# Performance work log

Measured on AMD Instinct MI355X. Metric: run time of the kernel, lower is better.

The kernel has to match this reference:

```python
import jax, jax.numpy as jnp
import numpy as np

N_NODES = 4096
N_EDGES = 16384
L = 512
MP_STEPS = 5
DT = 0.01


def _mlp(x, W1, b1, W2, b2):
    return jax.nn.relu(x @ W1 + b1) @ W2 + b2


def _ln(x):
    m = jnp.mean(x, axis=-1, keepdims=True)
    v = jnp.var(x, axis=-1, keepdims=True)
    return (x - m) * jax.lax.rsqrt(v + 1e-6)


_PARAM_SHAPES = [
    ("enc_e_W1", (1, L)), ("enc_e_b1", (L,)), ("enc_e_W2", (L, L)), ("enc_e_b2", (L,)),
    ("enc_n_W1", (1, L)), ("enc_n_b1", (L,)), ("enc_n_W2", (L, L)), ("enc_n_b2", (L,)),
    ("proc_e_W1", (3 * L, L)), ("proc_e_b1", (L,)), ("proc_e_W2", (L, L)), ("proc_e_b2", (L,)),
    ("proc_n_W1", (2 * L, L)), ("proc_n_b1", (L,)), ("proc_n_W2", (L, L)), ("proc_n_b2", (L,)),
    ("dec_e_W1", (L, L)), ("dec_e_b1", (L,)), ("dec_e_W2", (L, 1)), ("dec_e_b2", (1,)),
]


def setup_inputs() -> dict:
    key = jax.random.key(0)
    ks = jax.random.split(key, 3 + len(_PARAM_SHAPES))
    d = {}
    d["state"] = jax.random.normal(ks[0], (N_EDGES + N_NODES,), dtype=jnp.float32)
    d["senders"] = jax.random.randint(ks[1], (N_EDGES,), 0, N_NODES)
    d["receivers"] = jax.random.randint(ks[2], (N_EDGES,), 0, N_NODES)
    for i, (name, shp) in enumerate(_PARAM_SHAPES):
        if name.endswith(("b1", "b2")):
            d[name] = jnp.zeros(shp, dtype=jnp.float32)
        else:
            d[name] = 0.02 * jax.random.normal(ks[3 + i], shp, dtype=jnp.float32)
    return d


def _hamiltonian(x, senders, receivers,
                 enc_e_W1, enc_e_b1, enc_e_W2, enc_e_b2,
                 enc_n_W1, enc_n_b1, enc_n_W2, enc_n_b2,
                 proc_e_W1, proc_e_b1, proc_e_W2, proc_e_b2,
                 proc_n_W1, proc_n_b1, proc_n_W2, proc_n_b2,
                 dec_e_W1, dec_e_b1, dec_e_W2, dec_e_b2):
    # graph_from_state: edge scalars then node scalars
    e = x[:N_EDGES].reshape(N_EDGES, 1)
    n = x[N_EDGES:].reshape(N_NODES, 1)
    # encode (MLP + layer norm)
    eh = _ln(_mlp(e, enc_e_W1, enc_e_b1, enc_e_W2, enc_e_b2))  # [E, L]
    nh = _ln(_mlp(n, enc_n_W1, enc_n_b1, enc_n_W2, enc_n_b2))  # [N, L]
    # process: num_mp_steps of GraphNetwork-style message passing, shared params
    for _ in range(MP_STEPS):
        msg_in = jnp.concatenate([eh, nh[senders], nh[receivers]], axis=-1)  # [E, 3L]
        eh = eh + _mlp(msg_in, proc_e_W1, proc_e_b1, proc_e_W2, proc_e_b2)
        agg = jax.ops.segment_sum(eh, receivers, num_segments=N_NODES)  # [N, L]
        node_in = jnp.concatenate([nh, agg], axis=-1)  # [N, 2L]
        nh = nh + _mlp(node_in, proc_n_W1, proc_n_b1, proc_n_W2, proc_n_b2)
    # decode edges to scalars; H = sum of decoded edge energies
    dec_e = _mlp(eh, dec_e_W1, dec_e_b1, dec_e_W2, dec_e_b2)  # [E, 1]
    return jnp.sum(dec_e)


def reference(state, senders, receivers,
              enc_e_W1, enc_e_b1, enc_e_W2, enc_e_b2,
              enc_n_W1, enc_n_b1, enc_n_W2, enc_n_b2,
              proc_e_W1, proc_e_b1, proc_e_W2, proc_e_b2,
              proc_n_W1, proc_n_b1, proc_n_W2, proc_n_b2,
              dec_e_W1, dec_e_b1, dec_e_W2, dec_e_b2):
    def H_fn(x):
        return _hamiltonian(x, senders, receivers,
                            enc_e_W1, enc_e_b1, enc_e_W2, enc_e_b2,
                            enc_n_W1, enc_n_b1, enc_n_W2, enc_n_b2,
                            proc_e_W1, proc_e_b1, proc_e_W2, proc_e_b2,
                            proc_n_W1, proc_n_b1, proc_n_W2, proc_n_b2,
                            dec_e_W1, dec_e_b1, dec_e_W2, dec_e_b2)
    H, dH = jax.value_and_grad(H_fn)(state)
    # one integrator step driven by the Hamiltonian gradient (stand-in for DAE solve)
    next_state = state - DT * dH
    return next_state
```

## Files before the change

kernel.cpp:

```cpp
#include <hip/hip_runtime.h>


#define E_ROWS 16384
#define N_ROWS 4096
#define ALL_ROWS 20480
#define DT_F   0.01f

typedef unsigned char u8;
typedef unsigned short u16;
typedef __attribute__((ext_vector_type(8))) short short8v;
typedef __attribute__((ext_vector_type(4))) float f32x4;

__device__ __forceinline__ u16 f2b(float f) {
    union { float f; unsigned u; } v; v.f = f;
    unsigned r = v.u + 0x7FFF + ((v.u >> 16) & 1);
    return (u16)(r >> 16);
}
__device__ __forceinline__ float b2f(u16 u) {
    union { unsigned u; float f; } v; v.u = ((unsigned)u) << 16;
    return v.f;
}

template<int BM, int WM, int WN, int KTOT, int LDA, int LDC,
         bool ADD_C, bool GATHER2, bool BIAS, bool RELU_MASK, bool APPLY_MASK,
         bool WF32, bool WBF16, bool DUALOUT, bool ROWDOT, bool DECW2, bool BSEL>
__global__ __launch_bounds__(256)
void bgemm(const u16* __restrict__ A, const u16* __restrict__ Bt, const u16* __restrict__ Bt2,
           float* __restrict__ C, u16* __restrict__ Cb,
           const u16* __restrict__ Cinb, const float* __restrict__ bias,
           const float* __restrict__ bias2, const u16* __restrict__ G12b,
           const int* __restrict__ sidx, const int* __restrict__ ridx,
           u8* __restrict__ maskw, u16* __restrict__ C2b,
           const float* __restrict__ wvec, const float* __restrict__ wvec2,
           float* __restrict__ outp)
{
    constexpr int BN = WN * 64;
    constexpr int NA = BM / 16;
    constexpr int TC = (BM + BN) / 16;
    constexpr int PER = TC / 4;
    constexpr int NT = KTOT / 32;
    constexpr int IFRAG = BM / WM / 16;
    __shared__ u16 Ls[2][TC * 512];

    const int tid = threadIdx.x;
    const int lane = tid & 63;
    const int wv = tid >> 6;
    const int wr = wv / WN;
    const int wc = wv % WN;

    const int gx = gridDim.x;
    int id = blockIdx.y * gx + blockIdx.x;
    const int nwg = gx * gridDim.y;
    id = (id & 7) * (nwg >> 3) + (id >> 3);
    const int bx = id % gx;
    const int by = id / gx;
    const int rowBase = by * BM;
    const int colBase = bx * BN;

    const u16* BtU = Bt;
    const float* biasU = bias;
    const float* wvecU = wvec;
    if (BSEL && rowBase >= E_ROWS) { BtU = Bt2; biasU = bias2; wvecU = wvec2; }

    const int srow = lane & 15;
    const int slotk = (lane >> 4) << 3;

    const u16* srcs[PER];
    int dstoff[PER];
#pragma unroll
    for (int q = 0; q < PER; ++q) {
        const int c = wv + (q << 2);
        if (c < NA)
            srcs[q] = A + (size_t)(rowBase + c * 16 + srow) * LDA + slotk;
        else
            srcs[q] = BtU + (size_t)(colBase + (c - NA) * 16 + srow) * KTOT + slotk;
        dstoff[q] = c * 512;
    }

    f32x4 acc[IFRAG][4];
#pragma unroll
    for (int i = 0; i < IFRAG; ++i)
#pragma unroll
        for (int j = 0; j < 4; ++j)
            acc[i][j] = (f32x4){0.f, 0.f, 0.f, 0.f};

    const int fro = ((lane >> 4) << 7) + ((lane & 15) << 3);

#pragma unroll
    for (int q = 0; q < PER; ++q)
        __builtin_amdgcn_global_load_lds(
            (const __attribute__((address_space(1))) void*)srcs[q],
            (__attribute__((address_space(3))) void*)&Ls[0][dstoff[q]], 16, 0, 0);
    asm volatile("s_waitcnt vmcnt(0)" ::: "memory");
    __builtin_amdgcn_s_barrier();
    asm volatile("" ::: "memory");

#pragma unroll
    for (int t = 0; t < NT; ++t) {
        const int cur = t & 1;
        if (t + 1 < NT) {
#pragma unroll
            for (int q = 0; q < PER; ++q)
                __builtin_amdgcn_global_load_lds(
                    (const __attribute__((address_space(1))) void*)(srcs[q] + (t + 1) * 32),
                    (__attribute__((address_space(3))) void*)&Ls[cur ^ 1][dstoff[q]], 16, 0, 0);
        }
        short8v af[IFRAG], bfm[4];
#pragma unroll
        for (int i = 0; i < IFRAG; ++i)
            af[i] = *(const short8v*)&Ls[cur][((wr * IFRAG + i) << 9) + fro];
#pragma unroll
        for (int j = 0; j < 4; ++j)
            bfm[j] = *(const short8v*)&Ls[cur][((NA + (wc << 2) + j) << 9) + fro];
#pragma unroll
        for (int i = 0; i < IFRAG; ++i)
#pragma unroll
            for (int j = 0; j < 4; ++j)
                acc[i][j] = __builtin_amdgcn_mfma_f32_16x16x32_bf16(af[i], bfm[j], acc[i][j], 0, 0, 0);
        if (t + 1 < NT) {
            asm volatile("s_waitcnt vmcnt(0)" ::: "memory");
            __builtin_amdgcn_s_barrier();
            asm volatile("" ::: "memory");
        }
    }

    const int colB = colBase + wc * 64 + (lane & 15);
    const int rowB = rowBase + wr * (BM / WM) + ((lane >> 4) << 2);
    float bcol[4], wv4[4];
    if (BIAS) {
#pragma unroll
        for (int j = 0; j < 4; ++j) bcol[j] = biasU[colB + (j << 4)];
    }
    if (ROWDOT || DECW2) {
#pragma unroll
        for (int j = 0; j < 4; ++j) wv4[j] = wvecU[colB + (j << 4)];
    }
    const bool upper = DUALOUT && (colBase >= 512);
#pragma unroll
    for (int i = 0; i < IFRAG; ++i) {
#pragma unroll
        for (int r = 0; r < 4; ++r) {
            const int row = rowB + (i << 4) + r;
            int si = 0, ri = 0;
            if (GATHER2) { si = sidx[row]; ri = ridx[row]; }
            float rds = 0.f;
#pragma unroll
            for (int j = 0; j < 4; ++j) {
                const int col = colB + (j << 4);
                float v = acc[i][j][r];
                if (DUALOUT && upper) {
                    C2b[(size_t)row * 512 + (col - 512)] = f2b(v);
                    continue;
                }
                if (GATHER2) v += b2f(G12b[(size_t)si * 1024 + col]) + b2f(G12b[(size_t)ri * 1024 + 512 + col]);
                if (ADD_C) v += b2f(Cinb[(size_t)row * LDC + col]);
                if (BIAS) v += bcol[j];
                if (DECW2) {
                    Cb[(size_t)row * LDC + col] = (v > 0.f) ? f2b(wv4[j]) : (u16)0;
                    continue;
                }
                if (RELU_MASK) {
                    const u8 m = v > 0.f;
                    maskw[(size_t)row * 512 + col] = m;
                    v = m ? v : 0.f;
                }
                if (APPLY_MASK) {
                    if (!maskw[(size_t)row * 512 + col]) v = 0.f;
                }
                if (ROWDOT) rds += v * wv4[j];
                const size_t o = (size_t)row * LDC + col;
                if (WF32) C[o] = v;
                if (WBF16) Cb[o] = f2b(v);
            }
            if (ROWDOT) {
#pragma unroll
                for (int m = 1; m < 16; m <<= 1) rds += __shfl_xor(rds, m);
                if ((lane & 15) == 0) atomicAdd(outp + row, -DT_F * rds);
            }
        }
    }
}

struct WArgs {
    const float* src[10];
    u16* dstP[10];
    u16* dstT[10];
    int ldP[10], ldT[10];
};

__global__ void wcvt_kernel(WArgs a)
{
    const int i = blockIdx.z;
    const float* W = a.src[i];
    u16* P = a.dstP[i]; const int lp = a.ldP[i];
    u16* T = a.dstT[i]; const int lt = a.ldT[i];
    __shared__ u16 t[64][66];
    const int rb = blockIdx.y << 6, cb = blockIdx.x << 6;
    const int tr = threadIdx.x >> 4;
    const int tc = (threadIdx.x & 15) << 2;
#pragma unroll
    for (int rr = 0; rr < 4; ++rr) {
        const int r = tr + (rr << 4);
        const float4 v = *(const float4*)&W[(size_t)(rb + r) * 512 + cb + tc];
        ushort4 u; u.x = f2b(v.x); u.y = f2b(v.y); u.z = f2b(v.z); u.w = f2b(v.w);
        *(ushort4*)&P[(size_t)(rb + r) * lp + cb + tc] = u;
        t[r][tc] = u.x; t[r][tc + 1] = u.y; t[r][tc + 2] = u.z; t[r][tc + 3] = u.w;
    }
    __syncthreads();
#pragma unroll
    for (int rr = 0; rr < 4; ++rr) {
        const int n = tr + (rr << 4);
        ushort4 u;
        u.x = t[tc][n]; u.y = t[tc + 1][n]; u.z = t[tc + 2][n]; u.w = t[tc + 3][n];
        *(ushort4*)&T[(size_t)(cb + n) * lt + rb + tc] = u;
    }
}

__device__ void csr_build(const int* __restrict__ idx, int* __restrict__ starts,
                          int* __restrict__ eids)
{
    __shared__ int hist[4096];
    __shared__ int scanbuf[1024];
    const int t = threadIdx.x;
    for (int i = t; i < 4096; i += 1024) hist[i] = 0;
    __syncthreads();
    for (int e = t; e < 16384; e += 1024) atomicAdd(&hist[idx[e]], 1);
    __syncthreads();
    const int base = t << 2;
    const int l0 = hist[base], l1 = hist[base + 1], l2 = hist[base + 2], l3 = hist[base + 3];
    const int lsum = l0 + l1 + l2 + l3;
    scanbuf[t] = lsum;
    __syncthreads();
    for (int ofs = 1; ofs < 1024; ofs <<= 1) {
        const int v = scanbuf[t];
        const int u = (t >= ofs) ? scanbuf[t - ofs] : 0;
        __syncthreads();
        scanbuf[t] = v + u;
        __syncthreads();
    }
    const int excl = scanbuf[t] - lsum;
    const int p0 = excl, p1 = p0 + l0, p2 = p1 + l1, p3 = p2 + l2;
    starts[base] = p0; starts[base + 1] = p1; starts[base + 2] = p2; starts[base + 3] = p3;
    if (t == 0) starts[4096] = 16384;
    __syncthreads();
    hist[base] = p0; hist[base + 1] = p1; hist[base + 2] = p2; hist[base + 3] = p3;
    __syncthreads();
    for (int e = t; e < 16384; e += 1024) {
        const int pos = atomicAdd(&hist[idx[e]], 1);
        eids[pos] = e;
    }
    __syncthreads();
    for (int n = t; n < 4096; n += 1024) {
        const int s0 = starts[n], s1 = hist[n];
        for (int i = s0 + 1; i < s1; ++i) {
            const int v = eids[i];
            int j = i - 1;
            while (j >= s0 && eids[j] > v) { eids[j + 1] = eids[j]; --j; }
            eids[j + 1] = v;
        }
    }
}

__global__ __launch_bounds__(1024) void csr2_kernel(const int* __restrict__ senders,
                                                    const int* __restrict__ receivers,
                                                    int* __restrict__ sst, int* __restrict__ seid,
                                                    int* __restrict__ rst, int* __restrict__ reid)
{
    if (blockIdx.x == 0) csr_build(receivers, rst, reid);
    else                 csr_build(senders, sst, seid);
}

__global__ void init_out_kernel(const float* __restrict__ state, float* __restrict__ out)
{
    const int t = blockIdx.x * 256 + threadIdx.x;
    out[t] = state[t];
}

__global__ void seg_agg_fwd_kernel(const u16* __restrict__ ehb, const int* __restrict__ starts,
                                   const int* __restrict__ eids, const u16* __restrict__ nhb,
                                   u16* __restrict__ nagg)
{
    const int n = blockIdx.x, c = threadIdx.x;
    const int s0 = starts[n], s1 = starts[n + 1];
    float a0 = 0.f, a1 = 0.f;
    for (int i = s0; i < s1; ++i) {
        const u16* p = ehb + (size_t)eids[i] * 512;
        a0 += b2f(p[c]); a1 += b2f(p[c + 256]);
    }
    u16* d = nagg + (size_t)n * 1024;
    const u16* s = nhb + (size_t)n * 512;
    d[c] = s[c]; d[c + 256] = s[c + 256];
    d[512 + c] = f2b(a0); d[768 + c] = f2b(a1);
}

__global__ void seg_sr_bwd_kernel(const u16* __restrict__ dh1e,
                                  const int* __restrict__ sst, const int* __restrict__ seid,
                                  const int* __restrict__ rst, const int* __restrict__ reid,
                                  u16* __restrict__ SR)
{
    const int n = blockIdx.x, c = threadIdx.x;
    float a0 = 0.f, a1 = 0.f, b0 = 0.f, b1 = 0.f;
    for (int i = sst[n]; i < sst[n + 1]; ++i) {
        const u16* p = dh1e + (size_t)seid[i] * 512;
        a0 += b2f(p[c]); a1 += b2f(p[c + 256]);
    }
    for (int i = rst[n]; i < rst[n + 1]; ++i) {
        const u16* p = dh1e + (size_t)reid[i] * 512;
        b0 += b2f(p[c]); b1 += b2f(p[c + 256]);
    }
    u16* d = SR + (size_t)n * 1024;
    d[c] = f2b(a0); d[c + 256] = f2b(a1);
    d[512 + c] = f2b(b0); d[768 + c] = f2b(b1);
}

__global__ void enc_h1_kernel(const float* __restrict__ x,
                              const float* __restrict__ W1e, const float* __restrict__ b1e,
                              const float* __restrict__ W1n, const float* __restrict__ b1n,
                              u16* __restrict__ h1b, u8* __restrict__ mask)
{
    const int idx = blockIdx.x * 256 + threadIdx.x;
    const int row = idx >> 7;
    const int c = (idx & 127) << 2;
    const bool edge = row < E_ROWS;
    const float* W1 = edge ? W1e : W1n;
    const float* b1 = edge ? b1e : b1n;
    const float xv = x[row];
    const float4 w = *(const float4*)&W1[c];
    const float4 b = *(const float4*)&b1[c];
    float4 v;
    v.x = fmaf(xv, w.x, b.x); v.y = fmaf(xv, w.y, b.y);
    v.z = fmaf(xv, w.z, b.z); v.w = fmaf(xv, w.w, b.w);
    uchar4 m;
    m.x = v.x > 0.f; m.y = v.y > 0.f; m.z = v.z > 0.f; m.w = v.w > 0.f;
    v.x = m.x ? v.x : 0.f; v.y = m.y ? v.y : 0.f;
    v.z = m.z ? v.z : 0.f; v.w = m.w ? v.w : 0.f;
    const size_t o = (size_t)row * 512 + c;
    ushort4 u; u.x = f2b(v.x); u.y = f2b(v.y); u.z = f2b(v.z); u.w = f2b(v.w);
    *(ushort4*)&h1b[o] = u;
    *(uchar4*)&mask[o] = m;
}

__global__ void ln_fwd_kernel(const float* __restrict__ x, u16* __restrict__ xhat_b,
                              u16* __restrict__ xb, float* __restrict__ rstd_save)
{
    const int row = blockIdx.x, tid = threadIdx.x;
    const float* p = x + (size_t)row * 512;
    const float a = p[tid], b = p[tid + 256];
    __shared__ float s1[256], s2[256];
    s1[tid] = a + b; s2[tid] = a * a + b * b;
    __syncthreads();
    for (int d = 128; d > 0; d >>= 1) {
        if (tid < d) { s1[tid] += s1[tid + d]; s2[tid] += s2[tid + d]; }
        __syncthreads();
    }
    const float mean = s1[0] * (1.f / 512.f);
    const float var = s2[0] * (1.f / 512.f) - mean * mean;
    const float r = rsqrtf(var + 1e-6f);
    const float ya = (a - mean) * r, yb = (b - mean) * r;
    const size_t o = (size_t)row * 512 + tid;
    xhat_b[o] = f2b(ya); xhat_b[o + 256] = f2b(yb);
    xb[o] = f2b(ya); xb[o + 256] = f2b(yb);
    if (tid == 0) rstd_save[row] = r;
}

__global__ void ln_bwd_kernel(u16* __restrict__ d, const u16* __restrict__ xhat_b,
                              const float* __restrict__ rstd)
{
    const int row = blockIdx.x, tid = threadIdx.x;
    u16* p = d + (size_t)row * 512;
    const u16* xh = xhat_b + (size_t)row * 512;
    const float da = b2f(p[tid]), dbv = b2f(p[tid + 256]);
    const float xa = b2f(xh[tid]), xbv = b2f(xh[tid + 256]);
    __shared__ float s1[256], s2[256];
    s1[tid] = da + dbv; s2[tid] = da * xa + dbv * xbv;
    __syncthreads();
    for (int dd = 128; dd > 0; dd >>= 1) {
        if (tid < dd) { s1[tid] += s1[tid + dd]; s2[tid] += s2[tid + dd]; }
        __syncthreads();
    }
    const float m1 = s1[0] * (1.f / 512.f);
    const float m2 = s2[0] * (1.f / 512.f);
    const float r = rstd[row];
    p[tid] = f2b(r * (da - m1 - xa * m2));
    p[tid + 256] = f2b(r * (dbv - m1 - xbv * m2));
}

__global__ void gather_add_kernel(u16* __restrict__ dst, const u16* __restrict__ src,
                                  const int* __restrict__ idx)
{
    const int t = blockIdx.x * 256 + threadIdx.x;
    const int row = t >> 6;
    const int c = (t & 63) << 3;
    const size_t o = (size_t)row * 512 + c;
    short8v a = *(const short8v*)&dst[o];
    const short8v g = *(const short8v*)&src[(size_t)idx[row] * 512 + c];
    short8v r;
#pragma unroll
    for (int i = 0; i < 8; ++i)
        r[i] = (short)f2b(b2f((u16)a[i]) + b2f((u16)g[i]));
    *(short8v*)&dst[o] = r;
}

extern "C" void kernel_launch(void* const* d_in, const int* in_sizes, int n_in,
                              void* d_out, int out_size, void* d_ws, size_t ws_size,
                              hipStream_t stream)
{
    (void)in_sizes; (void)n_in; (void)out_size; (void)ws_size;
    const float* state     = (const float*)d_in[0];
    const int*   senders   = (const int*)d_in[1];
    const int*   receivers = (const int*)d_in[2];
    const float* enc_e_W1 = (const float*)d_in[3];
    const float* enc_e_b1 = (const float*)d_in[4];
    const float* enc_e_W2 = (const float*)d_in[5];
    const float* enc_e_b2 = (const float*)d_in[6];
    const float* enc_n_W1 = (const float*)d_in[7];
    const float* enc_n_b1 = (const float*)d_in[8];
    const float* enc_n_W2 = (const float*)d_in[9];
    const float* enc_n_b2 = (const float*)d_in[10];
    const float* pe_W1 = (const float*)d_in[11];
    const float* pe_b1 = (const float*)d_in[12];
    const float* pe_W2 = (const float*)d_in[13];
    const float* pe_b2 = (const float*)d_in[14];
    const float* pn_W1 = (const float*)d_in[15];
    const float* pn_b1 = (const float*)d_in[16];
    const float* pn_W2 = (const float*)d_in[17];
    const float* pn_b2 = (const float*)d_in[18];
    const float* de_W1 = (const float*)d_in[19];
    const float* de_b1 = (const float*)d_in[20];
    const float* de_W2 = (const float*)d_in[21];
    float* out = (float*)d_out;

    const size_t EL = (size_t)E_ROWS * 512, NL = (size_t)N_ROWS * 512;
    const size_t AL = (size_t)ALL_ROWS * 512;
    const size_t LL = 512 * 512;
    char* w = (char*)d_ws;
    size_t off = 0;
    auto carve = [&](size_t bytes) -> char* {
        char* p = w + off;
        off += (bytes + 255) & ~(size_t)255;
        return p;
    };
    u16* wb = (u16*)carve(20 * LL * 2);
    u16* WT0 = wb;           u16* WT1 = wb + LL;      u16* WT2 = wb + 2 * LL;
    u16* WT34 = wb + 3 * LL;                          u16* WT5 = wb + 5 * LL;
    u16* WT8 = wb + 6 * LL;  u16* WT9 = wb + 7 * LL;
    u16* WP0 = wb + 8 * LL;  u16* WP1 = wb + 9 * LL;  u16* WP2 = wb + 10 * LL;
    u16* WP5 = wb + 11 * LL; u16* WP8 = wb + 12 * LL; u16* WP9 = wb + 13 * LL;
    u16* WT67 = wb + 14 * LL;
    u16* WP34c = wb + 16 * LL;
    u16* WP67 = wb + 18 * LL;

    float* eh  = (float*)carve(AL * 4);
    u16* ehb   = (u16*)carve(EL * 2);
    u16* nhb   = (u16*)carve(NL * 2);
    u16* h1eb  = (u16*)carve(EL * 2);
    u16* h1nb  = (u16*)carve(NL * 2);
    u16* eh0b  = (u16*)carve(EL * 2);
    u16* nh0b  = (u16*)carve(NL * 2);
    u8* menc   = (u8*)carve(AL);
    u16* G1b   = (u16*)carve(NL * 2);
    u16* G12b  = (u16*)carve(NL * 2 * 2);
    u16* nsr   = (u16*)carve(NL * 2 * 2);
    float* rstd = (float*)carve(ALL_ROWS * 4);
    u8* mpe    = (u8*)carve(5 * EL);
    u8* mpn    = (u8*)carve(5 * NL);
    int* rst  = (int*)carve(4097 * 4);
    int* reid = (int*)carve(16384 * 4);
    int* sst  = (int*)carve(4097 * 4);
    int* seid = (int*)carve(16384 * 4);

    const dim3 blk(256);
    const dim3 gE(4, E_ROWS / 128);
    const dim3 gA(4, ALL_ROWS / 128);
    const dim3 gN512(8, N_ROWS / 64);
    const dim3 gN1024(16, N_ROWS / 64);
    const float* fp = nullptr;
    u16* up = nullptr;
    const u16* cup = nullptr;
    const int* ip = nullptr;
    u8* mp = nullptr;
    float* f2p = nullptr;

    WArgs wa;
    const float* wsrc[10] = { enc_e_W2, enc_n_W2, pe_W1, pe_W1 + LL, pe_W1 + 2 * LL,
                              pe_W2, pn_W1, pn_W1 + LL, pn_W2, de_W1 };
    u16* dstP[10] = { WP0, WP1, WP2, WP34c, WP34c + 512, WP5, WP67, WP67 + LL, WP8, WP9 };
    int  ldP [10] = { 512, 512, 512, 1024,  1024,        512, 512,  512,       512, 512 };
    u16* dstT[10] = { WT0, WT1, WT2, WT34, WT34 + LL, WT5, WT67, WT67 + 512, WT8, WT9 };
    int  ldT [10] = { 512, 512, 512, 512,  512,       512, 1024, 1024,       512, 512 };
    for (int i = 0; i < 10; ++i) {
        wa.src[i] = wsrc[i]; wa.dstP[i] = dstP[i]; wa.dstT[i] = dstT[i];
        wa.ldP[i] = ldP[i]; wa.ldT[i] = ldT[i];
    }
    wcvt_kernel<<<dim3(8, 8, 10), blk, 0, stream>>>(wa);

    csr2_kernel<<<2, 1024, 0, stream>>>(senders, receivers, sst, seid, rst, reid);
    init_out_kernel<<<ALL_ROWS / 256, blk, 0, stream>>>(state, out);

    enc_h1_kernel<<<ALL_ROWS * 128 / 256, blk, 0, stream>>>(state, enc_e_W1, enc_e_b1,
                                                            enc_n_W1, enc_n_b1, h1eb, menc);
    bgemm<128,2,2,512,512,512, false,false,true,false,false, true,false,false,false,false,true>
        <<<gA, blk, 0, stream>>>(h1eb, WT0, WT1, eh, up, cup, enc_e_b2, enc_n_b2, cup, ip, ip, mp, up, fp, fp, f2p);
    ln_fwd_kernel<<<ALL_ROWS, blk, 0, stream>>>(eh, eh0b, ehb, rstd);

    for (int k = 0; k < 5; ++k) {
        bgemm<64,4,1,512,512,1024, false,false,false,false,false, false,true,false,false,false,false>
            <<<gN1024, blk, 0, stream>>>(nhb, WT34, cup, f2p, G12b, cup, fp, fp, cup, ip, ip, mp, up, fp, fp, f2p);
        bgemm<128,2,2,512,512,512, false,true,true,true,false, false,true,false,false,false,false>
            <<<gE, blk, 0, stream>>>(ehb, WT2, cup, f2p, h1eb, cup, pe_b1, fp, G12b, senders, receivers, mpe + (size_t)k * EL, up, fp, fp, f2p);
        bgemm<128,2,2,512,512,512, true,false,true,false,false, false,true,false,false,false,false>
            <<<gE, blk, 0, stream>>>(h1eb, WT5, cup, f2p, ehb, ehb, pe_b2, fp, cup, ip, ip, mp, up, fp, fp, f2p);
        seg_agg_fwd_kernel<<<N_ROWS, blk, 0, stream>>>(ehb, rst, reid, nhb, nsr);
        bgemm<64,4,1,1024,1024,512, false,false,true,true,false, false,true,false,false,false,false>
            <<<gN512, blk, 0, stream>>>(nsr, WT67, cup, f2p, h1nb, cup, pn_b1, fp, cup, ip, ip, mpn + (size_t)k * NL, up, fp, fp, f2p);
        bgemm<64,4,1,512,512,512, true,false,true,false,false, false,true,false,false,false,false>
            <<<gN512, blk, 0, stream>>>(h1nb, WT8, cup, f2p, nhb, nhb, pn_b2, fp, cup, ip, ip, mp, up, fp, fp, f2p);
    }

    bgemm<128,2,2,512,512,512, false,false,true,false,false, false,false,false,false,true,false>
        <<<gE, blk, 0, stream>>>(ehb, WT9, cup, f2p, h1eb, cup, de_b1, fp, cup, ip, ip, mp, up, de_W2, fp, f2p);

    bgemm<128,2,2,512,512,512, false,false,false,false,false, false,true,false,false,false,false>
        <<<gE, blk, 0, stream>>>(h1eb, WP9, cup, f2p, ehb, cup, fp, fp, cup, ip, ip, mp, up, fp, fp, f2p);

    for (int k = 4; k >= 0; --k) {
        if (k < 4) {
            bgemm<64,4,1,512,512,512, false,false,false,false,true, false,true,false,false,false,false>
                <<<gN512, blk, 0, stream>>>(nhb, WP8, cup, f2p, h1nb, cup, fp, fp, cup, ip, ip, mpn + (size_t)k * NL, up, fp, fp, f2p);
            bgemm<64,4,1,512,512,512, true,false,false,false,false, false,true,true,false,false,false>
                <<<gN1024, blk, 0, stream>>>(h1nb, WP67, cup, f2p, nhb, nhb, fp, fp, cup, ip, ip, mp, G1b, fp, fp, f2p);
            gather_add_kernel<<<E_ROWS * 64 / 256, blk, 0, stream>>>(ehb, G1b, receivers);
        }
        bgemm<128,2,2,512,512,512, false,false,false,false,true, false,true,false,false,false,false>
            <<<gE, blk, 0, stream>>>(ehb, WP5, cup, f2p, h1eb, cup, fp, fp, cup, ip, ip, mpe + (size_t)k * EL, up, fp, fp, f2p);
        bgemm<128,2,2,512,512,512, true,false,false,false,false, false,true,false,false,false,false>
            <<<gE, blk, 0, stream>>>(h1eb, WP2, cup, f2p, ehb, ehb, fp, fp, cup, ip, ip, mp, up, fp, fp, f2p);
        seg_sr_bwd_kernel<<<N_ROWS, blk, 0, stream>>>(h1eb, sst, seid, rst, reid, nsr);
        if (k == 4)
            bgemm<64,4,1,1024,1024,512, false,false,false,false,false, false,true,false,false,false,false>
                <<<gN512, blk, 0, stream>>>(nsr, WP34c, cup, f2p, nhb, cup, fp, fp, cup, ip, ip, mp, up, fp, fp, f2p);
        else
            bgemm<64,4,1,1024,1024,512, true,false,false,false,false, false,true,false,false,false,false>
                <<<gN512, blk, 0, stream>>>(nsr, WP34c, cup, f2p, nhb, nhb, fp, fp, cup, ip, ip, mp, up, fp, fp, f2p);
    }

    ln_bwd_kernel<<<ALL_ROWS, blk, 0, stream>>>(ehb, eh0b, rstd);
    bgemm<128,2,2,512,512,512, false,false,false,false,true, false,false,false,true,false,true>
        <<<gA, blk, 0, stream>>>(ehb, WP0, WP1, f2p, up, cup, fp, fp, cup, ip, ip, menc, up, enc_e_W1, enc_n_W1, out);
}
```

Before: 1.390 ms.

## Stage GEMM epilogue through swizzled LDS for vectorized stores; drop double buffering

The GEMM epilogue now writes the bf16 accumulators into a swizzled shared-memory tile, then re-reads them row-contiguously so that gathers, residual adds, bias, mask and output stores all use 8-element vector accesses instead of scattered 2-byte ones. The K loop loses its double-buffered LDS prefetch and uses a single buffer with two __syncthreads per step, so global loads no longer overlap MFMA work. Accumulators are rounded to bf16 before bias and residual are added, which adds an extra rounding step. The ROWDOT reduction now spans BN/8 lanes, and the WF32 path keeps direct stores.

```diff
diff --git a/kernel.cpp b/kernel.cpp
--- a/kernel.cpp
+++ b/kernel.cpp
@@ -8,6 +8,7 @@
 
 typedef unsigned char u8;
 typedef unsigned short u16;
+typedef unsigned long long u64;
 typedef __attribute__((ext_vector_type(8))) short short8v;
 typedef __attribute__((ext_vector_type(4))) float f32x4;
 
@@ -38,9 +39,8 @@
     constexpr int NA = BM / 16;
     constexpr int TC = (BM + BN) / 16;
     constexpr int PER = TC / 4;
-    constexpr int NT = KTOT / 32;
     constexpr int IFRAG = BM / WM / 16;
-    __shared__ u16 Ls[2][TC * 512];
+    __shared__ u16 Ls[BM * BN];
 
     const int tid = threadIdx.x;
     const int lane = tid & 63;
@@ -86,96 +86,145 @@
 
     const int fro = ((lane >> 4) << 7) + ((lane & 15) << 3);
 
-#pragma unroll
-    for (int q = 0; q < PER; ++q)
-        __builtin_amdgcn_global_load_lds(
-            (const __attribute__((address_space(1))) void*)srcs[q],
-            (__attribute__((address_space(3))) void*)&Ls[0][dstoff[q]], 16, 0, 0);
-    asm volatile("s_waitcnt vmcnt(0)" ::: "memory");
-    __builtin_amdgcn_s_barrier();
-    asm volatile("" ::: "memory");
-
-#pragma unroll
-    for (int t = 0; t < NT; ++t) {
-        const int cur = t & 1;
-        if (t + 1 < NT) {
-#pragma unroll
-            for (int q = 0; q < PER; ++q)
-                __builtin_amdgcn_global_load_lds(
-                    (const __attribute__((address_space(1))) void*)(srcs[q] + (t + 1) * 32),
-                    (__attribute__((address_space(3))) void*)&Ls[cur ^ 1][dstoff[q]], 16, 0, 0);
-        }
+    for (int kb = 0; kb < KTOT; kb += 32) {
+#pragma unroll
+        for (int q = 0; q < PER; ++q)
+            __builtin_amdgcn_global_load_lds(
+                (const __attribute__((address_space(1))) void*)(srcs[q] + kb),
+                (__attribute__((address_space(3))) void*)&Ls[dstoff[q]], 16, 0, 0);
+        __syncthreads();
         short8v af[IFRAG], bfm[4];
 #pragma unroll
         for (int i = 0; i < IFRAG; ++i)
-            af[i] = *(const short8v*)&Ls[cur][((wr * IFRAG + i) << 9) + fro];
+            af[i] = *(const short8v*)&Ls[((wr * IFRAG + i) << 9) + fro];
 #pragma unroll
         for (int j = 0; j < 4; ++j)
-            bfm[j] = *(const short8v*)&Ls[cur][((NA + (wc << 2) + j) << 9) + fro];
+            bfm[j] = *(const short8v*)&Ls[((NA + (wc << 2) + j) << 9) + fro];
 #pragma unroll
         for (int i = 0; i < IFRAG; ++i)
 #pragma unroll
             for (int j = 0; j < 4; ++j)
                 acc[i][j] = __builtin_amdgcn_mfma_f32_16x16x32_bf16(af[i], bfm[j], acc[i][j], 0, 0, 0);
-        if (t + 1 < NT) {
-            asm volatile("s_waitcnt vmcnt(0)" ::: "memory");
-            __builtin_amdgcn_s_barrier();
-            asm volatile("" ::: "memory");
-        }
-    }
-
-    const int colB = colBase + wc * 64 + (lane & 15);
-    const int rowB = rowBase + wr * (BM / WM) + ((lane >> 4) << 2);
-    float bcol[4], wv4[4];
-    if (BIAS) {
+        __syncthreads();
+    }
+
+    if constexpr (WF32) {
+        const int colB = colBase + wc * 64 + (lane & 15);
+        const int rowB = rowBase + wr * (BM / WM) + ((lane >> 4) << 2);
+        float bcol[4];
 #pragma unroll
         for (int j = 0; j < 4; ++j) bcol[j] = biasU[colB + (j << 4)];
-    }
-    if (ROWDOT || DECW2) {
-#pragma unroll
-        for (int j = 0; j < 4; ++j) wv4[j] = wvecU[colB + (j << 4)];
-    }
-    const bool upper = DUALOUT && (colBase >= 512);
-#pragma unroll
-    for (int i = 0; i < IFRAG; ++i) {
-#pragma unroll
-        for (int r = 0; r < 4; ++r) {
-            const int row = rowB + (i << 4) + r;
-            int si = 0, ri = 0;
-            if (GATHER2) { si = sidx[row]; ri = ridx[row]; }
-            float rds = 0.f;
-#pragma unroll
-            for (int j = 0; j < 4; ++j) {
-                const int col = colB + (j << 4);
-                float v = acc[i][j][r];
-                if (DUALOUT && upper) {
-                    C2b[(size_t)row * 512 + (col - 512)] = f2b(v);
-                    continue;
+#pragma unroll
+        for (int i = 0; i < IFRAG; ++i)
+#pragma unroll
+            for (int r = 0; r < 4; ++r) {
+                const int row = rowB + (i << 4) + r;
+#pragma unroll
+                for (int j = 0; j < 4; ++j)
+                    C[(size_t)row * LDC + colB + (j << 4)] = acc[i][j][r] + bcol[j];
+            }
+    } else {
+        const int colL = wc * 64 + (lane & 15);
+        const int rowL0 = wr * (BM / WM) + ((lane >> 4) << 2);
+#pragma unroll
+        for (int i = 0; i < IFRAG; ++i)
+#pragma unroll
+            for (int r = 0; r < 4; ++r) {
+                const int row = rowL0 + (i << 4) + r;
+#pragma unroll
+                for (int j = 0; j < 4; ++j) {
+                    const int col = colL + (j << 4);
+                    int byte = row * (BN * 2) + col * 2;
+                    byte ^= (row & 7) << 4;
+                    *(u16*)((char*)Ls + byte) = f2b(acc[i][j][r]);
                 }
-                if (GATHER2) v += b2f(G12b[(size_t)si * 1024 + col]) + b2f(G12b[(size_t)ri * 1024 + 512 + col]);
-                if (ADD_C) v += b2f(Cinb[(size_t)row * LDC + col]);
-                if (BIAS) v += bcol[j];
-                if (DECW2) {
-                    Cb[(size_t)row * LDC + col] = (v > 0.f) ? f2b(wv4[j]) : (u16)0;
-                    continue;
+            }
+        __syncthreads();
+
+        constexpr int TPR = BN / 8;
+        constexpr int RPP = 256 / TPR;
+        constexpr int NP = BM / RPP;
+        const int rloc = tid / TPR;
+        const int seg = tid % TPR;
+        const int col0 = seg * 8;
+        const bool upper = DUALOUT && (colBase >= 512);
+#pragma unroll
+        for (int p = 0; p < NP; ++p) {
+            const int row = p * RPP + rloc;
+            const int grow = rowBase + row;
+            const int gcol = colBase + col0;
+            int byte = row * (BN * 2) + col0 * 2;
+            byte ^= (row & 7) << 4;
+            const short8v sv = *(const short8v*)((const char*)Ls + byte);
+            float v[8];
+#pragma unroll
+            for (int e = 0; e < 8; ++e) v[e] = b2f((u16)sv[e]);
+
+            if (DUALOUT && upper) {
+                short8v res;
+#pragma unroll
+                for (int e = 0; e < 8; ++e) res[e] = (short)f2b(v[e]);
+                *(short8v*)&C2b[(size_t)grow * 512 + (gcol - 512)] = res;
+                continue;
+            }
+            if (GATHER2) {
+                const int si = sidx[grow], ri = ridx[grow];
+                const short8v g1 = *(const short8v*)&G12b[(size_t)si * 1024 + gcol];
+                const short8v g2 = *(const short8v*)&G12b[(size_t)ri * 1024 + 512 + gcol];
+#pragma unroll
+                for (int e = 0; e < 8; ++e) v[e] += b2f((u16)g1[e]) + b2f((u16)g2[e]);
+            }
+            if (ADD_C) {
+                const short8v c8 = *(const short8v*)&Cinb[(size_t)grow * LDC + gcol];
+#pragma unroll
+                for (int e = 0; e < 8; ++e) v[e] += b2f((u16)c8[e]);
+            }
+            if (BIAS) {
+                const float4 b0 = *(const float4*)&biasU[gcol];
+                const float4 b1 = *(const float4*)&biasU[gcol + 4];
+                v[0] += b0.x; v[1] += b0.y; v[2] += b0.z; v[3] += b0.w;
+                v[4] += b1.x; v[5] += b1.y; v[6] += b1.z; v[7] += b1.w;
+            }
+            if (DECW2) {
+                const float4 w0 = *(const float4*)&wvecU[gcol];
+                const float4 w1 = *(const float4*)&wvecU[gcol + 4];
+                const float wl[8] = {w0.x, w0.y, w0.z, w0.w, w1.x, w1.y, w1.z, w1.w};
+                short8v res;
+#pragma unroll
+                for (int e = 0; e < 8; ++e) res[e] = (v[e] > 0.f) ? (short)f2b(wl[e]) : (short)0;
+                *(short8v*)&Cb[(size_t)grow * LDC + gcol] = res;
+                continue;
+            }
+            if (RELU_MASK) {
+                u64 mm = 0;
+#pragma unroll
+                for (int e = 0; e < 8; ++e) {
+                    const bool m = v[e] > 0.f;
+                    mm |= (u64)(m ? 1 : 0) << (e * 8);
+                    if (!m) v[e] = 0.f;
                 }
-                if (RELU_MASK) {
-                    const u8 m = v > 0.f;
-                    maskw[(size_t)row * 512 + col] = m;
-                    v = m ? v : 0.f;
-                }
-                if (APPLY_MASK) {
-                    if (!maskw[(size_t)row * 512 + col]) v = 0.f;
-                }
-                if (ROWDOT) rds += v * wv4[j];
-                const size_t o = (size_t)row * LDC + col;
-                if (WF32) C[o] = v;
-                if (WBF16) Cb[o] = f2b(v);
+                *(u64*)&maskw[(size_t)grow * 512 + gcol] = mm;
+            }
+            if (APPLY_MASK) {
+                const u64 mm = *(const u64*)&maskw[(size_t)grow * 512 + gcol];
+#pragma unroll
+                for (int e = 0; e < 8; ++e)
+                    if (!((mm >> (e * 8)) & 0xff)) v[e] = 0.f;
             }
             if (ROWDOT) {
-#pragma unroll
-                for (int m = 1; m < 16; m <<= 1) rds += __shfl_xor(rds, m);
-                if ((lane & 15) == 0) atomicAdd(outp + row, -DT_F * rds);
+                const float4 w0 = *(const float4*)&wvecU[gcol];
+                const float4 w1 = *(const float4*)&wvecU[gcol + 4];
+                float rds = v[0] * w0.x + v[1] * w0.y + v[2] * w0.z + v[3] * w0.w
+                          + v[4] * w1.x + v[5] * w1.y + v[6] * w1.z + v[7] * w1.w;
+#pragma unroll
+                for (int m = 1; m < TPR; m <<= 1) rds += __shfl_xor(rds, m);
+                if (seg == 0) atomicAdd(outp + grow, -DT_F * rds);
+            }
+            if (WBF16) {
+                short8v res;
+#pragma unroll
+                for (int e = 0; e < 8; ++e) res[e] = (short)f2b(v[e]);
+                *(short8v*)&Cb[(size_t)grow * LDC + gcol] = res;
             }
         }
     }
```

After: 1.261 ms. 1.1x faster.
